# Kernel optimization log

Hardware: AMD Instinct MI355X
Metric: run time of the kernel (lower is better)

## Reference

```python
import jax, jax.numpy as jnp
import numpy as np

FACTOR = 1.0
KERNEL = 3
PAD = 1
STRIDE = 1


def setup_inputs() -> dict:
    key = jax.random.key(0)
    ks = jax.random.split(key, 7)
    B_, Cin, Cout, L, CODE = 32, 128, 128, 4096, 2
    return {
        "input": jax.random.normal(ks[0], (B_, Cin, L), dtype=jnp.float32),
        "codes": jax.random.normal(ks[1], (B_, CODE, CODE), dtype=jnp.float32),
        "weight": jax.random.normal(ks[2], (Cout, Cin, KERNEL), dtype=jnp.float32) * 0.05,
        "A": jax.random.normal(ks[3], (Cin, CODE, KERNEL), dtype=jnp.float32) * 0.05,
        "B": jax.random.normal(ks[4], (Cout, CODE, KERNEL), dtype=jnp.float32) * 0.05,
        "bias": jax.random.normal(ks[5], (Cout,), dtype=jnp.float32) * 0.05,
        "bias_context": jax.random.normal(ks[6], (CODE, Cout), dtype=jnp.float32) * 0.05,
    }


def reference(input, codes, weight, A, B, bias, bias_context):
    # Hypernetwork-generated per-sample conv weights (low-rank via codes)
    w = jnp.einsum('ick,bcr->birk', A, codes)            # (b, in, code, k)
    context_w = jnp.einsum('birk,ork->boik', w, B)       # (b, out, in, k)
    combined_weight = weight + FACTOR * context_w        # (b, out, in, k)

    diag = jnp.diagonal(codes, axis1=-2, axis2=-1)       # (b, code)
    context_bias = diag @ bias_context                   # (b, out)
    combined_bias = bias + FACTOR * context_bias         # (b, out)

    # circular padding along spatial axis
    padded = jnp.pad(input, ((0, 0), (0, 0), (PAD, PAD)), mode='wrap')
    L_out = (input.shape[-1] + 2 * PAD - KERNEL) // STRIDE + 1
    # windowed view: (b, in, L_out, k) via k shifted slices (k is tiny, loop ok)
    windows = jnp.stack([padded[:, :, j:j + L_out * STRIDE:STRIDE] for j in range(KERNEL)], axis=-1)
    out = jnp.einsum('bihw,boiw->boh', windows, combined_weight)
    return out + combined_bias[..., None]
```

## Files before the change

kernel.cpp:

```cpp
#include <hip/hip_runtime.h>
#include <hip/hip_bf16.h>
#include <stdint.h>
#include <stddef.h>

#define L_LEN 4096
#define CIN   128
#define COUT  128
#define NB    32
#define KTOT  384
#define TN    64
#define TPB   4
#define ROWS  (TN + 2)

typedef __bf16 bf16x8 __attribute__((ext_vector_type(8)));
typedef float  f32x4  __attribute__((ext_vector_type(4)));

__device__ __forceinline__ uint16_t f2bf(float f) {
    union { float f; uint32_t u; } v; v.f = f;
    return (uint16_t)((v.u + 0x7fffu + ((v.u >> 16) & 1u)) >> 16);
}
__device__ __forceinline__ uint32_t pack2(float lo, float hi) {
    return (uint32_t)f2bf(lo) | ((uint32_t)f2bf(hi) << 16);
}

__global__ __launch_bounds__(256) void geps_combine(
    const float* __restrict__ codes, const float* __restrict__ weight,
    const float* __restrict__ Amat,  const float* __restrict__ Bmat,
    const float* __restrict__ bias,  const float* __restrict__ bias_ctx,
    uint16_t* __restrict__ Wc, float* __restrict__ cbias)
{
    int tid = blockIdx.x * 256 + threadIdx.x;
    if (tid < NB * COUT * KTOT) {
        int j    = tid & 7;
        int lane = (tid >> 3) & 63;
        int mt   = (tid >> 9) & 1;
        int tmp  = tid >> 10;
        int t    = tmp % 12;
        int bo   = tmp / 12;
        int og   = bo & 3;
        int b    = bo >> 2;
        int col  = t * 32 + (lane >> 4) * 8 + j;
        int k    = col >> 7;
        int i    = col & 127;
        int o    = og * 32 + mt * 16 + (lane & 15);
        float cw = 0.f;
        #pragma unroll
        for (int c = 0; c < 2; ++c) {
            float a = Amat[i * 6 + c * 3 + k];
            #pragma unroll
            for (int r = 0; r < 2; ++r)
                cw += a * codes[b * 4 + c * 2 + r] * Bmat[o * 6 + r * 3 + k];
        }
        float val = weight[o * 384 + i * 3 + k] + cw;
        Wc[tid] = f2bf(val);
    }
    if (tid < NB * COUT) {
        int b = tid >> 7, o = tid & 127;
        float cb = bias[o];
        #pragma unroll
        for (int c = 0; c < 2; ++c)
            cb += codes[b * 4 + c * 2 + c] * bias_ctx[c * 128 + o];
        cbias[tid] = cb;
    }
}


#define LOAD_HALF(IT, H0)                                                    \
    {                                                                        \
        int L_p4 = ((IT) << 4) + (tid >> 4);                                 \
        int L_qd = tid & 15;                                                 \
        const float* L_r0 = inb + (size_t)(4 * L_p4) * L_LEN + (H0) + 4 * L_qd; \
        st[0] = *(const float4*)(L_r0);                                      \
        st[1] = *(const float4*)(L_r0 + L_LEN);                              \
        st[2] = *(const float4*)(L_r0 + 2 * L_LEN);                          \
        st[3] = *(const float4*)(L_r0 + 3 * L_LEN);                          \
        if ((IT) && tid < 128) {                                             \
            int L_p    = tid & 63;                                           \
            int L_side = tid >> 6;                                           \
            int L_r    = L_side ? (ROWS - 1) : 0;                            \
            int L_gh   = ((H0) - 1 + L_r) & (L_LEN - 1);                     \
            hx0 = inb[(size_t)(2 * L_p) * L_LEN + L_gh];                     \
            hx1 = inb[(size_t)(2 * L_p + 1) * L_LEN + L_gh];                 \
        }                                                                    \
    }

#define PACK_HALF(IT, XP)                                                    \
    {                                                                        \
        uint16_t* P_Xw = (XP);                                               \
        int P_p4 = ((IT) << 4) + (tid >> 4);                                 \
        int P_qd = tid & 15;                                                 \
        const int P_off = (4 * P_p4) & 7;                                    \
        const int P_pc  = P_p4 >> 1;                                         \
        _Pragma("unroll")                                                    \
        for (int P_j4 = 0; P_j4 < 4; ++P_j4) {                               \
            int P_r  = 1 + 4 * P_qd + P_j4;                                  \
            int P_ch = P_pc ^ (P_r & 15);                                    \
            uint2 P_w;                                                       \
            P_w.x = pack2(((const float*)&st[0])[P_j4],                      \
                          ((const float*)&st[1])[P_j4]);                     \
            P_w.y = pack2(((const float*)&st[2])[P_j4],                      \
                          ((const float*)&st[3])[P_j4]);                     \
            *(uint2*)&P_Xw[P_r * 128 + (P_ch << 3) + P_off] = P_w;           \
        }                                                                    \
        if ((IT) && tid < 128) {                                             \
            int P_p     = tid & 63;                                          \
            int P_side  = tid >> 6;                                          \
            int P_hr    = P_side ? (ROWS - 1) : 0;                           \
            int P_chunk = (P_p >> 2) ^ (P_hr & 15);                          \
            *(uint32_t*)&P_Xw[P_hr * 128 + (P_chunk << 3) + ((2 * P_p) & 7)] = \
                pack2(hx0, hx1);                                             \
        }                                                                    \
    }

__global__ __launch_bounds__(256, 2) void geps_conv(
    const float* __restrict__ in, const uint16_t* __restrict__ Wc,
    const float* __restrict__ cbias, float* __restrict__ out)
{
    __shared__ uint16_t __attribute__((aligned(16))) Xt[2][ROWS * 128];
    __shared__ float cb[COUT];

    const int tid  = threadIdx.x;
    const int d    = blockIdx.x;
    const int b    = 4 * (d & 7) + (d >> 7);
    const int hb   = ((d >> 3) & 15) * (TN * TPB);
    const int lane = tid & 63;
    const int wid  = tid >> 6;
    const int m16  = lane & 15;
    const int q    = lane >> 4;
    const int mq   = wid * 32;

    if (tid < COUT) cb[tid] = cbias[b * COUT + tid];

    const float* inb = in + (size_t)b * CIN * L_LEN;
    const uint16_t* WcW = Wc + (size_t)(b * 4 + wid) * 12288 + lane * 8;

    float4 st[4];
    float  hx0 = 0.f, hx1 = 0.f;
    f32x4  acc[2][4];

    LOAD_HALF(0, hb)
    PACK_HALF(0, &Xt[0][0])
    LOAD_HALF(1, hb)
    PACK_HALF(1, &Xt[0][0])
    __syncthreads();

    #pragma unroll 1
    for (int j = 0; j < TPB; ++j) {
        const int h0 = hb + j * TN;
        uint16_t* Xcur = &Xt[j & 1][0];
        uint16_t* Xnxt = &Xt[(j + 1) & 1][0];
        const bool pre = (j + 1 < TPB);

        if (pre) LOAD_HALF(0, h0 + TN)
        asm volatile("" ::: "memory");

        #pragma unroll
        for (int a = 0; a < 2; ++a)
            #pragma unroll
            for (int c = 0; c < 4; ++c) acc[a][c] = 0.0f;

        bf16x8 ar[3][2];
        ar[0][0] = *(const bf16x8*)(WcW);
        ar[0][1] = *(const bf16x8*)(WcW + 512);
        ar[1][0] = *(const bf16x8*)(WcW + 1024);
        ar[1][1] = *(const bf16x8*)(WcW + 1536);

        #pragma unroll
        for (int t = 0; t < 12; ++t) {
            if (t + 2 < 12) {
                ar[(t + 2) % 3][0] = *(const bf16x8*)(WcW + (t + 2) * 1024);
                ar[(t + 2) % 3][1] = *(const bf16x8*)(WcW + (t + 2) * 1024 + 512);
            }
            if (t == 6 && pre) {
                PACK_HALF(0, Xnxt)
                LOAD_HALF(1, h0 + TN)
                asm volatile("" ::: "memory");
            }
            const int k   = t >> 2;
            const int i0c = (t & 3) << 2;
            bf16x8 bfv[4];
            #pragma unroll
            for (int nt = 0; nt < 4; ++nt) {
                int r  = nt * 16 + m16 + k;
                int ch = (i0c + q) ^ (r & 15);
                bfv[nt] = *(const bf16x8*)&Xcur[r * 128 + (ch << 3)];
            }
            #pragma unroll
            for (int nt = 0; nt < 4; ++nt) {
                acc[0][nt] = __builtin_amdgcn_mfma_f32_16x16x32_bf16(
                    ar[t % 3][0], bfv[nt], acc[0][nt], 0, 0, 0);
                acc[1][nt] = __builtin_amdgcn_mfma_f32_16x16x32_bf16(
                    ar[t % 3][1], bfv[nt], acc[1][nt], 0, 0, 0);
            }
        }

        float* outb = out + (size_t)b * COUT * L_LEN + h0;
        #pragma unroll
        for (int mt = 0; mt < 2; ++mt) {
            #pragma unroll
            for (int reg = 0; reg < 4; ++reg) {
                int o = mq + mt * 16 + q * 4 + reg;
                float bv = cb[o];
                float* orow = outb + (size_t)o * L_LEN;
                #pragma unroll
                for (int nt = 0; nt < 4; ++nt)
                    __builtin_nontemporal_store(acc[mt][nt][reg] + bv,
                                                &orow[nt * 16 + m16]);
            }
        }

        if (pre) PACK_HALF(1, Xnxt)
        __syncthreads();
    }
}

extern "C" void kernel_launch(void* const* d_in, const int* in_sizes, int n_in,
                              void* d_out, int out_size, void* d_ws, size_t ws_size,
                              hipStream_t stream) {
    const float* input    = (const float*)d_in[0];
    const float* codes    = (const float*)d_in[1];
    const float* weight   = (const float*)d_in[2];
    const float* Amat     = (const float*)d_in[3];
    const float* Bmat     = (const float*)d_in[4];
    const float* bias     = (const float*)d_in[5];
    const float* bias_ctx = (const float*)d_in[6];
    float* out = (float*)d_out;

    uint16_t* Wc    = (uint16_t*)d_ws;
    float*    cbias = (float*)((char*)d_ws + (size_t)NB * COUT * KTOT * 2);

    geps_combine<<<dim3((NB * COUT * KTOT) / 256), 256, 0, stream>>>(
        codes, weight, Amat, Bmat, bias, bias_ctx, Wc, cbias);
    geps_conv<<<dim3(NB * L_LEN / (TN * TPB)), 256, 0, stream>>>(
        input, Wc, cbias, out);
}
```

Measured before the change: 144.8 us.

## Split conv work into single-tile 128-thread blocks over output-channel halves

The conv kernel no longer loops over four consecutive spatial tiles with a double-buffered LDS pipeline. Each block now handles one 64-wide tile and half of the output channels with 2 waves, and the grid grows to 4096 blocks. The aim is more blocks in flight and higher occupancy, with the cross-iteration pipeline replaced by plain parallelism. In exchange, each input tile is loaded and packed twice (once per output-channel half), and per-block prologue costs are no longer amortised across tiles.

```diff
diff --git a/kernel.cpp b/kernel.cpp
--- a/kernel.cpp
+++ b/kernel.cpp
@@ -9,7 +9,6 @@
 #define NB    32
 #define KTOT  384
 #define TN    64
-#define TPB   4
 #define ROWS  (TN + 2)
 
 typedef __bf16 bf16x8 __attribute__((ext_vector_type(8)));
@@ -65,29 +64,20 @@
 }
 
 
-#define LOAD_HALF(IT, H0)                                                    \
+#define LOADQ(C, SB)                                                         \
     {                                                                        \
-        int L_p4 = ((IT) << 4) + (tid >> 4);                                 \
+        int L_p4 = ((C) << 3) + (tid >> 4);                                  \
         int L_qd = tid & 15;                                                 \
-        const float* L_r0 = inb + (size_t)(4 * L_p4) * L_LEN + (H0) + 4 * L_qd; \
-        st[0] = *(const float4*)(L_r0);                                      \
-        st[1] = *(const float4*)(L_r0 + L_LEN);                              \
-        st[2] = *(const float4*)(L_r0 + 2 * L_LEN);                          \
-        st[3] = *(const float4*)(L_r0 + 3 * L_LEN);                          \
-        if ((IT) && tid < 128) {                                             \
-            int L_p    = tid & 63;                                           \
-            int L_side = tid >> 6;                                           \
-            int L_r    = L_side ? (ROWS - 1) : 0;                            \
-            int L_gh   = ((H0) - 1 + L_r) & (L_LEN - 1);                     \
-            hx0 = inb[(size_t)(2 * L_p) * L_LEN + L_gh];                     \
-            hx1 = inb[(size_t)(2 * L_p + 1) * L_LEN + L_gh];                 \
-        }                                                                    \
-    }
-
-#define PACK_HALF(IT, XP)                                                    \
+        const float* L_r0 = inb + (size_t)(4 * L_p4) * L_LEN + h0 + 4 * L_qd; \
+        (SB)[0] = *(const float4*)(L_r0);                                    \
+        (SB)[1] = *(const float4*)(L_r0 + L_LEN);                            \
+        (SB)[2] = *(const float4*)(L_r0 + 2 * L_LEN);                        \
+        (SB)[3] = *(const float4*)(L_r0 + 3 * L_LEN);                        \
+    }
+
+#define PACKQ(C, SB)                                                         \
     {                                                                        \
-        uint16_t* P_Xw = (XP);                                               \
-        int P_p4 = ((IT) << 4) + (tid >> 4);                                 \
+        int P_p4 = ((C) << 3) + (tid >> 4);                                  \
         int P_qd = tid & 15;                                                 \
         const int P_off = (4 * P_p4) & 7;                                    \
         const int P_pc  = P_p4 >> 1;                                         \
@@ -96,121 +86,118 @@
             int P_r  = 1 + 4 * P_qd + P_j4;                                  \
             int P_ch = P_pc ^ (P_r & 15);                                    \
             uint2 P_w;                                                       \
-            P_w.x = pack2(((const float*)&st[0])[P_j4],                      \
-                          ((const float*)&st[1])[P_j4]);                     \
-            P_w.y = pack2(((const float*)&st[2])[P_j4],                      \
-                          ((const float*)&st[3])[P_j4]);                     \
-            *(uint2*)&P_Xw[P_r * 128 + (P_ch << 3) + P_off] = P_w;           \
+            P_w.x = pack2(((const float*)&(SB)[0])[P_j4],                    \
+                          ((const float*)&(SB)[1])[P_j4]);                   \
+            P_w.y = pack2(((const float*)&(SB)[2])[P_j4],                    \
+                          ((const float*)&(SB)[3])[P_j4]);                   \
+            *(uint2*)&Xt[P_r * 128 + (P_ch << 3) + P_off] = P_w;             \
         }                                                                    \
-        if ((IT) && tid < 128) {                                             \
-            int P_p     = tid & 63;                                          \
-            int P_side  = tid >> 6;                                          \
-            int P_hr    = P_side ? (ROWS - 1) : 0;                           \
-            int P_chunk = (P_p >> 2) ^ (P_hr & 15);                          \
-            *(uint32_t*)&P_Xw[P_hr * 128 + (P_chunk << 3) + ((2 * P_p) & 7)] = \
-                pack2(hx0, hx1);                                             \
-        }                                                                    \
-    }
-
-__global__ __launch_bounds__(256, 2) void geps_conv(
+    }
+
+__global__ __launch_bounds__(128, 3) void geps_conv(
     const float* __restrict__ in, const uint16_t* __restrict__ Wc,
     const float* __restrict__ cbias, float* __restrict__ out)
 {
-    __shared__ uint16_t __attribute__((aligned(16))) Xt[2][ROWS * 128];
-    __shared__ float cb[COUT];
+    __shared__ uint16_t __attribute__((aligned(16))) Xt[ROWS * 128];
+    __shared__ float cb[64];
 
     const int tid  = threadIdx.x;
     const int d    = blockIdx.x;
-    const int b    = 4 * (d & 7) + (d >> 7);
-    const int hb   = ((d >> 3) & 15) * (TN * TPB);
+    const int xcd  = d & 7;
+    const int dm   = d >> 3;
+    const int og   = dm & 1;
+    const int ht   = (dm >> 1) & 63;
+    const int b    = 4 * xcd + (dm >> 7);
+    const int h0   = ht * TN;
     const int lane = tid & 63;
-    const int wid  = tid >> 6;
+    const int w    = tid >> 6;
     const int m16  = lane & 15;
     const int q    = lane >> 4;
-    const int mq   = wid * 32;
-
-    if (tid < COUT) cb[tid] = cbias[b * COUT + tid];
+    const int og32 = og * 2 + w;
+
+    if (tid < 64) cb[tid] = cbias[b * COUT + og * 64 + tid];
 
     const float* inb = in + (size_t)b * CIN * L_LEN;
-    const uint16_t* WcW = Wc + (size_t)(b * 4 + wid) * 12288 + lane * 8;
-
-    float4 st[4];
-    float  hx0 = 0.f, hx1 = 0.f;
-    f32x4  acc[2][4];
-
-    LOAD_HALF(0, hb)
-    PACK_HALF(0, &Xt[0][0])
-    LOAD_HALF(1, hb)
-    PACK_HALF(1, &Xt[0][0])
+    const uint16_t* WcW = Wc + (size_t)(b * 4 + og32) * 12288 + lane * 8;
+
+    float4 st[2][4];
+    float  hx0, hx1;
+    {
+        int L_p    = tid & 63;
+        int L_side = tid >> 6;
+        int L_r    = L_side ? (ROWS - 1) : 0;
+        int L_gh   = (h0 - 1 + L_r) & (L_LEN - 1);
+        hx0 = inb[(size_t)(2 * L_p) * L_LEN + L_gh];
+        hx1 = inb[(size_t)(2 * L_p + 1) * L_LEN + L_gh];
+    }
+    LOADQ(0, st[0])
+    #pragma unroll
+    for (int c = 0; c < 4; ++c) {
+        if (c < 3) LOADQ(c + 1, st[(c + 1) & 1])
+        asm volatile("" ::: "memory");
+        PACKQ(c, st[c & 1])
+    }
+    {
+        int P_p     = tid & 63;
+        int P_side  = tid >> 6;
+        int P_hr    = P_side ? (ROWS - 1) : 0;
+        int P_chunk = (P_p >> 2) ^ (P_hr & 15);
+        *(uint32_t*)&Xt[P_hr * 128 + (P_chunk << 3) + ((2 * P_p) & 7)] =
+            pack2(hx0, hx1);
+    }
+
     __syncthreads();
 
-    #pragma unroll 1
-    for (int j = 0; j < TPB; ++j) {
-        const int h0 = hb + j * TN;
-        uint16_t* Xcur = &Xt[j & 1][0];
-        uint16_t* Xnxt = &Xt[(j + 1) & 1][0];
-        const bool pre = (j + 1 < TPB);
-
-        if (pre) LOAD_HALF(0, h0 + TN)
-        asm volatile("" ::: "memory");
-
-        #pragma unroll
-        for (int a = 0; a < 2; ++a)
+    f32x4 acc[2][4];
+    #pragma unroll
+    for (int a = 0; a < 2; ++a)
+        #pragma unroll
+        for (int cc = 0; cc < 4; ++cc) acc[a][cc] = 0.0f;
+
+    bf16x8 ar[3][2];
+    ar[0][0] = *(const bf16x8*)(WcW);
+    ar[0][1] = *(const bf16x8*)(WcW + 512);
+    ar[1][0] = *(const bf16x8*)(WcW + 1024);
+    ar[1][1] = *(const bf16x8*)(WcW + 1536);
+
+    #pragma unroll
+    for (int t = 0; t < 12; ++t) {
+        if (t + 2 < 12) {
+            ar[(t + 2) % 3][0] = *(const bf16x8*)(WcW + (t + 2) * 1024);
+            ar[(t + 2) % 3][1] = *(const bf16x8*)(WcW + (t + 2) * 1024 + 512);
+        }
+        const int k   = t >> 2;
+        const int i0c = (t & 3) << 2;
+        bf16x8 bfv[4];
+        #pragma unroll
+        for (int nt = 0; nt < 4; ++nt) {
+            int r  = nt * 16 + m16 + k;
+            int ch = (i0c + q) ^ (r & 15);
+            bfv[nt] = *(const bf16x8*)&Xt[r * 128 + (ch << 3)];
+        }
+        #pragma unroll
+        for (int nt = 0; nt < 4; ++nt) {
+            acc[0][nt] = __builtin_amdgcn_mfma_f32_16x16x32_bf16(
+                ar[t % 3][0], bfv[nt], acc[0][nt], 0, 0, 0);
+            acc[1][nt] = __builtin_amdgcn_mfma_f32_16x16x32_bf16(
+                ar[t % 3][1], bfv[nt], acc[1][nt], 0, 0, 0);
+        }
+    }
+
+    float* outb = out + (size_t)b * COUT * L_LEN + h0;
+    #pragma unroll
+    for (int mt = 0; mt < 2; ++mt) {
+        #pragma unroll
+        for (int reg = 0; reg < 4; ++reg) {
+            int o_loc = 32 * w + mt * 16 + q * 4 + reg;
+            int o     = og * 64 + o_loc;
+            float bv  = cb[o_loc];
+            float* orow = outb + (size_t)o * L_LEN;
             #pragma unroll
-            for (int c = 0; c < 4; ++c) acc[a][c] = 0.0f;
-
-        bf16x8 ar[3][2];
-        ar[0][0] = *(const bf16x8*)(WcW);
-        ar[0][1] = *(const bf16x8*)(WcW + 512);
-        ar[1][0] = *(const bf16x8*)(WcW + 1024);
-        ar[1][1] = *(const bf16x8*)(WcW + 1536);
-
-        #pragma unroll
-        for (int t = 0; t < 12; ++t) {
-            if (t + 2 < 12) {
-                ar[(t + 2) % 3][0] = *(const bf16x8*)(WcW + (t + 2) * 1024);
-                ar[(t + 2) % 3][1] = *(const bf16x8*)(WcW + (t + 2) * 1024 + 512);
-            }
-            if (t == 6 && pre) {
-                PACK_HALF(0, Xnxt)
-                LOAD_HALF(1, h0 + TN)
-                asm volatile("" ::: "memory");
-            }
-            const int k   = t >> 2;
-            const int i0c = (t & 3) << 2;
-            bf16x8 bfv[4];
-            #pragma unroll
-            for (int nt = 0; nt < 4; ++nt) {
-                int r  = nt * 16 + m16 + k;
-                int ch = (i0c + q) ^ (r & 15);
-                bfv[nt] = *(const bf16x8*)&Xcur[r * 128 + (ch << 3)];
-            }
-            #pragma unroll
-            for (int nt = 0; nt < 4; ++nt) {
-                acc[0][nt] = __builtin_amdgcn_mfma_f32_16x16x32_bf16(
-                    ar[t % 3][0], bfv[nt], acc[0][nt], 0, 0, 0);
-                acc[1][nt] = __builtin_amdgcn_mfma_f32_16x16x32_bf16(
-                    ar[t % 3][1], bfv[nt], acc[1][nt], 0, 0, 0);
-            }
-        }
-
-        float* outb = out + (size_t)b * COUT * L_LEN + h0;
-        #pragma unroll
-        for (int mt = 0; mt < 2; ++mt) {
-            #pragma unroll
-            for (int reg = 0; reg < 4; ++reg) {
-                int o = mq + mt * 16 + q * 4 + reg;
-                float bv = cb[o];
-                float* orow = outb + (size_t)o * L_LEN;
-                #pragma unroll
-                for (int nt = 0; nt < 4; ++nt)
-                    __builtin_nontemporal_store(acc[mt][nt][reg] + bv,
-                                                &orow[nt * 16 + m16]);
-            }
-        }
-
-        if (pre) PACK_HALF(1, Xnxt)
-        __syncthreads();
+            for (int nt = 0; nt < 4; ++nt)
+                __builtin_nontemporal_store(acc[mt][nt][reg] + bv,
+                                            &orow[nt * 16 + m16]);
+        }
     }
 }
 
@@ -231,6 +218,6 @@
 
     geps_combine<<<dim3((NB * COUT * KTOT) / 256), 256, 0, stream>>>(
         codes, weight, Amat, Bmat, bias, bias_ctx, Wc, cbias);
-    geps_conv<<<dim3(NB * L_LEN / (TN * TPB)), 256, 0, stream>>>(
+    geps_conv<<<dim3(NB * (L_LEN / TN) * 2), 128, 0, stream>>>(
         input, Wc, cbias, out);
 }
```

New measurement: 143.1 us. About the same (-1.2%).

## Stage per-sample conv weights in LDS and double the time tiles per block

Applied to the files above, without the earlier changes.

Each wave now copies its full bf16 weight slice into LDS once, using direct global-to-LDS loads. The inner MFMA loop then reads the A operand from LDS instead of re-fetching it from global memory for every output tile. TPB doubles to 8, so each block covers more tiles and amortizes that staging; the block-to-batch mapping is reorganized by XCD. The input prefetch now loads both halves up front and packs them after compute, and the end-of-tile barrier waits only on LDS counters so outstanding global loads are not drained. The roughly 130 KB of LDS per block limits each CU to one resident block and halves the grid, which reduces latency hiding.

```diff
diff --git a/kernel.cpp b/kernel.cpp
--- a/kernel.cpp
+++ b/kernel.cpp
@@ -9,7 +9,7 @@
 #define NB    32
 #define KTOT  384
 #define TN    64
-#define TPB   4
+#define TPB   8
 #define ROWS  (TN + 2)
 
 typedef __bf16 bf16x8 __attribute__((ext_vector_type(8)));
@@ -22,6 +22,15 @@
 __device__ __forceinline__ uint32_t pack2(float lo, float hi) {
     return (uint32_t)f2bf(lo) | ((uint32_t)f2bf(hi) << 16);
 }
+
+__device__ __forceinline__ void gll16(const void* g, void* l) {
+    __builtin_amdgcn_global_load_lds(
+        (const __attribute__((address_space(1))) void*)g,
+        (__attribute__((address_space(3))) void*)l, 16, 0, 0);
+}
+
+#define BARRIER_NODRAIN() \
+    asm volatile("s_waitcnt lgkmcnt(0)\n\ts_barrier" ::: "memory")
 
 __global__ __launch_bounds__(256) void geps_combine(
     const float* __restrict__ codes, const float* __restrict__ weight,
@@ -70,10 +79,10 @@
         int L_p4 = ((IT) << 4) + (tid >> 4);                                 \
         int L_qd = tid & 15;                                                 \
         const float* L_r0 = inb + (size_t)(4 * L_p4) * L_LEN + (H0) + 4 * L_qd; \
-        st[0] = *(const float4*)(L_r0);                                      \
-        st[1] = *(const float4*)(L_r0 + L_LEN);                              \
-        st[2] = *(const float4*)(L_r0 + 2 * L_LEN);                          \
-        st[3] = *(const float4*)(L_r0 + 3 * L_LEN);                          \
+        st[IT][0] = *(const float4*)(L_r0);                                  \
+        st[IT][1] = *(const float4*)(L_r0 + L_LEN);                          \
+        st[IT][2] = *(const float4*)(L_r0 + 2 * L_LEN);                      \
+        st[IT][3] = *(const float4*)(L_r0 + 3 * L_LEN);                      \
         if ((IT) && tid < 128) {                                             \
             int L_p    = tid & 63;                                           \
             int L_side = tid >> 6;                                           \
@@ -96,10 +105,10 @@
             int P_r  = 1 + 4 * P_qd + P_j4;                                  \
             int P_ch = P_pc ^ (P_r & 15);                                    \
             uint2 P_w;                                                       \
-            P_w.x = pack2(((const float*)&st[0])[P_j4],                      \
-                          ((const float*)&st[1])[P_j4]);                     \
-            P_w.y = pack2(((const float*)&st[2])[P_j4],                      \
-                          ((const float*)&st[3])[P_j4]);                     \
+            P_w.x = pack2(((const float*)&st[IT][0])[P_j4],                  \
+                          ((const float*)&st[IT][1])[P_j4]);                 \
+            P_w.y = pack2(((const float*)&st[IT][2])[P_j4],                  \
+                          ((const float*)&st[IT][3])[P_j4]);                 \
             *(uint2*)&P_Xw[P_r * 128 + (P_ch << 3) + P_off] = P_w;           \
         }                                                                    \
         if ((IT) && tid < 128) {                                             \
@@ -116,66 +125,63 @@
     const float* __restrict__ in, const uint16_t* __restrict__ Wc,
     const float* __restrict__ cbias, float* __restrict__ out)
 {
+    __shared__ uint16_t __attribute__((aligned(16))) ALds[4 * 12 * 1024];
     __shared__ uint16_t __attribute__((aligned(16))) Xt[2][ROWS * 128];
     __shared__ float cb[COUT];
 
     const int tid  = threadIdx.x;
     const int d    = blockIdx.x;
-    const int b    = 4 * (d & 7) + (d >> 7);
-    const int hb   = ((d >> 3) & 15) * (TN * TPB);
+    const int xcd  = d & 7;
+    const int b    = 4 * xcd + ((d >> 3) & 3);
+    const int hb   = (d >> 5) * (TN * TPB);
     const int lane = tid & 63;
     const int wid  = tid >> 6;
     const int m16  = lane & 15;
     const int q    = lane >> 4;
     const int mq   = wid * 32;
 
+    const float* inb = in + (size_t)b * CIN * L_LEN;
+
+    float4 st[2][4];
+    float  hx0 = 0.f, hx1 = 0.f;
+
+    LOAD_HALF(0, hb)
+    LOAD_HALF(1, hb)
+    {
+        const uint16_t* gsrc = Wc + (size_t)(b * 4 + wid) * 12288 + lane * 8;
+        uint16_t* ldst = &ALds[wid * 12288];
+        #pragma unroll
+        for (int n = 0; n < 24; ++n)
+            gll16(gsrc + n * 512, ldst + n * 512);
+    }
     if (tid < COUT) cb[tid] = cbias[b * COUT + tid];
-
-    const float* inb = in + (size_t)b * CIN * L_LEN;
-    const uint16_t* WcW = Wc + (size_t)(b * 4 + wid) * 12288 + lane * 8;
-
-    float4 st[4];
-    float  hx0 = 0.f, hx1 = 0.f;
-    f32x4  acc[2][4];
-
-    LOAD_HALF(0, hb)
     PACK_HALF(0, &Xt[0][0])
-    LOAD_HALF(1, hb)
     PACK_HALF(1, &Xt[0][0])
     __syncthreads();
 
+    f32x4 acc[2][4];
+    int cur = 0;
+
     #pragma unroll 1
     for (int j = 0; j < TPB; ++j) {
-        const int h0 = hb + j * TN;
-        uint16_t* Xcur = &Xt[j & 1][0];
-        uint16_t* Xnxt = &Xt[(j + 1) & 1][0];
+        const int h0  = hb + j * TN;
         const bool pre = (j + 1 < TPB);
 
-        if (pre) LOAD_HALF(0, h0 + TN)
+        if (pre) { LOAD_HALF(0, h0 + TN) LOAD_HALF(1, h0 + TN) }
         asm volatile("" ::: "memory");
 
         #pragma unroll
         for (int a = 0; a < 2; ++a)
             #pragma unroll
-            for (int c = 0; c < 4; ++c) acc[a][c] = 0.0f;
-
-        bf16x8 ar[3][2];
-        ar[0][0] = *(const bf16x8*)(WcW);
-        ar[0][1] = *(const bf16x8*)(WcW + 512);
-        ar[1][0] = *(const bf16x8*)(WcW + 1024);
-        ar[1][1] = *(const bf16x8*)(WcW + 1536);
+            for (int cc = 0; cc < 4; ++cc) acc[a][cc] = 0.0f;
+
+        const uint16_t* Xc = &Xt[cur][0];
+        const uint16_t* Aw = &ALds[wid * 12288 + lane * 8];
 
         #pragma unroll
         for (int t = 0; t < 12; ++t) {
-            if (t + 2 < 12) {
-                ar[(t + 2) % 3][0] = *(const bf16x8*)(WcW + (t + 2) * 1024);
-                ar[(t + 2) % 3][1] = *(const bf16x8*)(WcW + (t + 2) * 1024 + 512);
-            }
-            if (t == 6 && pre) {
-                PACK_HALF(0, Xnxt)
-                LOAD_HALF(1, h0 + TN)
-                asm volatile("" ::: "memory");
-            }
+            bf16x8 a0 = *(const bf16x8*)(Aw + t * 1024);
+            bf16x8 a1 = *(const bf16x8*)(Aw + t * 1024 + 512);
             const int k   = t >> 2;
             const int i0c = (t & 3) << 2;
             bf16x8 bfv[4];
@@ -183,16 +189,18 @@
             for (int nt = 0; nt < 4; ++nt) {
                 int r  = nt * 16 + m16 + k;
                 int ch = (i0c + q) ^ (r & 15);
-                bfv[nt] = *(const bf16x8*)&Xcur[r * 128 + (ch << 3)];
+                bfv[nt] = *(const bf16x8*)&Xc[r * 128 + (ch << 3)];
             }
             #pragma unroll
             for (int nt = 0; nt < 4; ++nt) {
                 acc[0][nt] = __builtin_amdgcn_mfma_f32_16x16x32_bf16(
-                    ar[t % 3][0], bfv[nt], acc[0][nt], 0, 0, 0);
+                    a0, bfv[nt], acc[0][nt], 0, 0, 0);
                 acc[1][nt] = __builtin_amdgcn_mfma_f32_16x16x32_bf16(
-                    ar[t % 3][1], bfv[nt], acc[1][nt], 0, 0, 0);
+                    a1, bfv[nt], acc[1][nt], 0, 0, 0);
             }
         }
+
+        if (pre) { PACK_HALF(0, &Xt[cur ^ 1][0]) PACK_HALF(1, &Xt[cur ^ 1][0]) }
 
         float* outb = out + (size_t)b * COUT * L_LEN + h0;
         #pragma unroll
@@ -209,8 +217,8 @@
             }
         }
 
-        if (pre) PACK_HALF(1, Xnxt)
-        __syncthreads();
+        BARRIER_NODRAIN();
+        cur ^= 1;
     }
 }
 
@@ -231,6 +239,6 @@
 
     geps_combine<<<dim3((NB * COUT * KTOT) / 256), 256, 0, stream>>>(
         codes, weight, Amat, Bmat, bias, bias_ctx, Wc, cbias);
-    geps_conv<<<dim3(NB * L_LEN / (TN * TPB)), 256, 0, stream>>>(
+    geps_conv<<<dim3(NB * (L_LEN / (TN * TPB))), 256, 0, stream>>>(
         input, Wc, cbias, out);
 }
```

Result: no change. 144.0 us (-0.6%).
